# Optimization experiments

Hardware: AMD Instinct MI355X
Metric: run time of the kernel (lower is better)

Reference implementation:

```python
import jax, jax.numpy as jnp
import numpy as np

EPS = 1e-6

def feature_map(x):
    # 'elu' feature map: elu(x) + 1 (positive feature map from Katharopoulos et al.)
    return jax.nn.elu(x) + 1.0

def setup_inputs() -> dict:
    key = jax.random.key(0)
    kq, kk, kv = jax.random.split(key, 3)
    B, L, H, D = 4, 2048, 16, 64
    q = jax.random.normal(kq, (B, L, H, D), dtype=jnp.float32)
    k = jax.random.normal(kk, (B, L, H, D), dtype=jnp.float32)
    v = jax.random.normal(kv, (B, L, H, D), dtype=jnp.float32)
    return {"q": q, "k": k, "v": v}

def reference(q, k, v):
    # q, k, v: [N, L, H, D]  (attention_mask=None -> causal linear attention)
    qf = feature_map(q)
    kf = feature_map(k)
    # normalizer: z[n,l,h] = sum_d qf[n,l,h,d] * cumsum_s<=l kf[n,s,h,d]
    z = jnp.einsum('nlhd,nlhd->nlh', qf, jnp.cumsum(kf, axis=1)) + EPS
    # causal_dot_product via scan over sequence with carry S[n,h,d,m]
    B, L, H, D = q.shape
    M = v.shape[-1]
    qs = jnp.moveaxis(qf, 1, 0)  # [L, N, H, D]
    ks = jnp.moveaxis(kf, 1, 0)
    vs = jnp.moveaxis(v, 1, 0)

    def step(S, qkv):
        ql, kl, vl = qkv                              # [N,H,D], [N,H,D], [N,H,M]
        S = S + jnp.einsum('nhd,nhm->nhdm', kl, vl)   # running sum of k v^T
        out = jnp.einsum('nhd,nhdm->nhm', ql, S)
        return S, out

    S0 = jnp.zeros((B, H, D, M), dtype=q.dtype)
    _, outs = jax.lax.scan(step, S0, (qs, ks, vs))    # outs: [L, N, H, M]
    v_ = jnp.moveaxis(outs, 0, 1)                     # [N, L, H, M]
    return v_ / z[..., None]
```

## Files before the change

kernel.cpp:

```cpp
#include <hip/hip_runtime.h>
#include <cstdint>

#define LL 2048
#define HH 16
#define DD 64
#define LSTR 1024
#define EPSF 1e-6f
#define PAD 72

typedef __bf16 bf16x8 __attribute__((ext_vector_type(8)));
typedef float floatx4 __attribute__((ext_vector_type(4)));
typedef unsigned short ushortx8 __attribute__((ext_vector_type(8)));
typedef unsigned short ushortx4 __attribute__((ext_vector_type(4)));
typedef unsigned short ushortx2 __attribute__((ext_vector_type(2)));

static __device__ __forceinline__ float fmap(float x){ return x > 0.f ? x + 1.f : __expf(x); }
static __device__ __forceinline__ unsigned short f2bf(float f){
    unsigned u = __builtin_bit_cast(unsigned, f);
    u += 0x7fffu + ((u >> 16) & 1u);
    return (unsigned short)(u >> 16);
}
static __device__ __forceinline__ float bf2f(unsigned short s){
    unsigned u = ((unsigned)s) << 16;
    return __builtin_bit_cast(float, u);
}
static __device__ __forceinline__ bf16x8 ldf(const unsigned short* p){
    return __builtin_bit_cast(bf16x8, *(const ushortx8*)p);
}
static __device__ __forceinline__ float4 fmap4(float4 a){
    return float4{fmap(a.x), fmap(a.y), fmap(a.z), fmap(a.w)};
}

template<bool MAP>
static __device__ __forceinline__ void st_sd(unsigned short* base, int r, int c, float4 a, float4 b){
    if (MAP) {
        *(ushortx4*)(base + r*PAD + c)     = ushortx4{ f2bf(fmap(a.x)), f2bf(fmap(a.y)), f2bf(fmap(a.z)), f2bf(fmap(a.w)) };
        *(ushortx4*)(base + (r+1)*PAD + c) = ushortx4{ f2bf(fmap(b.x)), f2bf(fmap(b.y)), f2bf(fmap(b.z)), f2bf(fmap(b.w)) };
    } else {
        *(ushortx4*)(base + r*PAD + c)     = ushortx4{ f2bf(a.x), f2bf(a.y), f2bf(a.z), f2bf(a.w) };
        *(ushortx4*)(base + (r+1)*PAD + c) = ushortx4{ f2bf(b.x), f2bf(b.y), f2bf(b.z), f2bf(b.w) };
    }
}
template<bool MAP>
static __device__ __forceinline__ void st_tr(unsigned short* base, int r, int c, float4 a, float4 b){
    float aa[4] = {a.x, a.y, a.z, a.w}, bb[4] = {b.x, b.y, b.z, b.w};
#pragma unroll
    for (int e = 0; e < 4; ++e) {
        float x0 = MAP ? fmap(aa[e]) : aa[e];
        float x1 = MAP ? fmap(bb[e]) : bb[e];
        *(ushortx2*)(base + (c+e)*PAD + r) = ushortx2{ f2bf(x0), f2bf(x1) };
    }
}

__global__ __launch_bounds__(256) void kA(const float* __restrict__ kp, const float* __restrict__ vp,
                                          float* __restrict__ qkv, float* __restrict__ ksq)
{
    __shared__ __align__(16) unsigned short kft[2][DD*PAD];
    __shared__ __align__(16) unsigned short vtt[2][DD*PAD];
    const int blk = blockIdx.x;
    const int bh = blk >> 3, oct = blk & 7, b = bh >> 4, h = bh & 15;
    const int t = threadIdx.x;
    const int w = t >> 6, lane = t & 63, quad = lane >> 4, lr = lane & 15;
    const int m0 = 16*w;

    floatx4 acc[4];
#pragma unroll
    for (int dt = 0; dt < 4; ++dt) acc[dt] = floatx4{0.f,0.f,0.f,0.f};
    float ksa = 0.f;

    const int64_t gb0 = ((int64_t)(b*LL + oct*256)*HH + h)*DD;
#pragma unroll
    for (int ii = 0; ii < 2; ++ii) {
        int flat = t + 256*ii;
        int l0s = (flat >> 4) * 2, col4 = (flat & 15) << 2;
        const float* gk = kp + gb0 + (int64_t)l0s*LSTR + col4;
        const float* gv = vp + gb0 + (int64_t)l0s*LSTR + col4;
        float4 ka = *(const float4*)gk, kb = *(const float4*)(gk + LSTR);
        float4 va = *(const float4*)gv, vb = *(const float4*)(gv + LSTR);
        st_tr<true >(kft[0], l0s, col4, ka, kb);
        st_tr<false>(vtt[0], l0s, col4, va, vb);
    }
    __syncthreads();

#pragma unroll
    for (int sc = 0; sc < 4; ++sc) {
        const int p = sc & 1;
        float4 ka[2], kb[2], va[2], vb[2];
        if (sc < 3) {
            const int64_t gb = gb0 + (int64_t)(sc+1)*DD*LSTR;
#pragma unroll
            for (int ii = 0; ii < 2; ++ii) {
                int flat = t + 256*ii;
                int l0s = (flat >> 4) * 2, col4 = (flat & 15) << 2;
                const float* gk = kp + gb + (int64_t)l0s*LSTR + col4;
                const float* gv = vp + gb + (int64_t)l0s*LSTR + col4;
                ka[ii] = *(const float4*)gk; kb[ii] = *(const float4*)(gk + LSTR);
                va[ii] = *(const float4*)gv; vb[ii] = *(const float4*)(gv + LSTR);
            }
        }
#pragma unroll
        for (int kk = 0; kk < 2; ++kk) {
            bf16x8 a = ldf(vtt[p] + (m0+lr)*PAD + kk*32 + quad*8);
#pragma unroll
            for (int dt = 0; dt < 4; ++dt) {
                bf16x8 bbf = ldf(kft[p] + (dt*16+lr)*PAD + kk*32 + quad*8);
                acc[dt] = __builtin_amdgcn_mfma_f32_16x16x32_bf16(a, bbf, acc[dt], 0, 0, 0);
            }
        }
        if (t < DD) {
#pragma unroll
            for (int jj = 0; jj < 8; ++jj) {
                ushortx8 u = *(const ushortx8*)(kft[p] + t*PAD + jj*8);
#pragma unroll
                for (int e = 0; e < 8; ++e) ksa += bf2f(u[e]);
            }
        }
        if (sc < 3) {
#pragma unroll
            for (int ii = 0; ii < 2; ++ii) {
                int flat = t + 256*ii;
                int l0s = (flat >> 4) * 2, col4 = (flat & 15) << 2;
                st_tr<true >(kft[p^1], l0s, col4, ka[ii], kb[ii]);
                st_tr<false>(vtt[p^1], l0s, col4, va[ii], vb[ii]);
            }
        }
        __syncthreads();
    }

    float* qo = qkv + (int64_t)blk*4096;
#pragma unroll
    for (int dt = 0; dt < 4; ++dt)
#pragma unroll
        for (int r = 0; r < 4; ++r)
            qo[(m0 + quad*4 + r)*DD + dt*16 + lr] = acc[dt][r];
    if (t < DD) ksq[(int64_t)blk*DD + t] = ksa;
}

__global__ __launch_bounds__(512, 4) void kM(const float* __restrict__ qp, const float* __restrict__ kp,
                                             const float* __restrict__ vp,
                                             const float* __restrict__ qkv, const float* __restrict__ ksq,
                                             float* __restrict__ outp)
{
    __shared__ __align__(16) unsigned short qf [DD*PAD];
    __shared__ __align__(16) unsigned short kfx[DD*PAD];
    __shared__ __align__(16) unsigned short kft[DD*PAD];
    __shared__ __align__(16) unsigned short vtt[DD*PAD];
    __shared__ __align__(16) unsigned short sld[DD*PAD];
    __shared__ __align__(16) unsigned short sct[DD*PAD];
    __shared__ __align__(16) unsigned short kpx[16*PAD];
    __shared__ float ksum[DD];
    __shared__ float zp2[2][DD];

    const int bid = blockIdx.x;
    const int bh = bid >> 3, oct = bid & 7, b = bh >> 4, h = bh & 15;
    const int t = threadIdx.x;
    const int w = t >> 6, lane = t & 63, quad = lane >> 4, lr = lane & 15;
    const int wi = w >> 1, wj = w & 1;
    const int l0 = 16*wi;
    const int l0s = (t >> 4) * 2, col4 = (t & 15) << 2;

    const int64_t bhb = ((int64_t)b*LL*HH + h)*DD;
    const int cg0 = oct*4;

    if (t < 135) *(ushortx8*)(kpx + PAD + t*8) = ushortx8{0,0,0,0,0,0,0,0};
    const int no = oct;
    if (t < DD) {
        float s = 0.f;
        for (int o = 0; o < no; ++o) s += ksq[((int64_t)bh*8 + o)*DD + t];
        ksum[t] = s;
        kpx[t] = f2bf(s);
    }
    floatx4 S_acc[2];
    S_acc[0] = floatx4{0.f,0.f,0.f,0.f};
    S_acc[1] = floatx4{0.f,0.f,0.f,0.f};
    for (int o = 0; o < no; ++o) {
        const float* qo = qkv + ((int64_t)bh*8 + o)*4096;
#pragma unroll
        for (int dtl = 0; dtl < 2; ++dtl)
#pragma unroll
            for (int r = 0; r < 4; ++r)
                S_acc[dtl][r] += qo[(l0 + quad*4 + r)*DD + 32*wj + dtl*16 + lr];
    }
#pragma unroll
    for (int dtl = 0; dtl < 2; ++dtl)
#pragma unroll
        for (int r = 0; r < 4; ++r)
            sld[(l0 + quad*4 + r)*PAD + 32*wj + dtl*16 + lr] = f2bf(S_acc[dtl][r]);

    {
        const int64_t gb = bhb + (int64_t)cg0*DD*LSTR;
        const float* gq = qp + gb + (int64_t)l0s*LSTR + col4;
        const float* gk = kp + gb + (int64_t)l0s*LSTR + col4;
        const float* gv = vp + gb + (int64_t)l0s*LSTR + col4;
        float4 q0 = *(const float4*)gq, q1 = *(const float4*)(gq + LSTR);
        float4 k0 = *(const float4*)gk, k1 = *(const float4*)(gk + LSTR);
        float4 v0 = *(const float4*)gv, v1 = *(const float4*)(gv + LSTR);
        st_sd<true >(qf , l0s, col4, q0, q1);
        st_sd<true >(kfx, l0s, col4, k0, k1);
        st_tr<true >(kft, l0s, col4, k0, k1);
        st_tr<false>(vtt, l0s, col4, v0, v1);
    }
    __syncthreads();

    float4 lk0 = float4{0,0,0,0}, lk1 = float4{0,0,0,0};
    float4 lv0 = float4{0,0,0,0}, lv1 = float4{0,0,0,0};

#pragma unroll 2
    for (int c = 0; c < 4; ++c) {
        const int cg = cg0 + c;
        float4 nq0, nq1, nk0, nk1, nv0, nv1;
        if (c < 3) {
            const int64_t gb = bhb + (int64_t)(cg+1)*DD*LSTR;
            const float* gq = qp + gb + (int64_t)l0s*LSTR + col4;
            const float* gk = kp + gb + (int64_t)l0s*LSTR + col4;
            const float* gv = vp + gb + (int64_t)l0s*LSTR + col4;
            nq0 = *(const float4*)gq; nq1 = *(const float4*)(gq + LSTR);
            nk0 = *(const float4*)gk; nk1 = *(const float4*)(gk + LSTR);
            nv0 = *(const float4*)gv; nv1 = *(const float4*)(gv + LSTR);
        }
        if (c > 0) {
            st_tr<false>(kft, l0s, col4, lk0, lk1);
            st_tr<false>(vtt, l0s, col4, lv0, lv1);
        }
        bf16x8 aq0 = ldf(qf + (l0+lr)*PAD + quad*8);
        bf16x8 aq1 = ldf(qf + (l0+lr)*PAD + 32 + quad*8);
        bf16x8 bsf[2][2];
#pragma unroll
        for (int kk = 0; kk < 2; ++kk)
#pragma unroll
            for (int mt = 0; mt < 2; ++mt)
                bsf[kk][mt] = ldf(sld + ((2*wj+mt)*16+lr)*PAD + kk*32 + quad*8);
        floatx4 s0 = floatx4{0.f,0.f,0.f,0.f}, s1 = floatx4{0.f,0.f,0.f,0.f}, sp = floatx4{0.f,0.f,0.f,0.f};
#pragma unroll
        for (int kk = 0; kk < 2; ++kk) {
            bf16x8 aqk = kk ? aq1 : aq0;
            bf16x8 b0 = ldf(kfx + ((2*wj+0)*16+lr)*PAD + kk*32 + quad*8);
            bf16x8 b1 = ldf(kfx + ((2*wj+1)*16+lr)*PAD + kk*32 + quad*8);
            s0 = __builtin_amdgcn_mfma_f32_16x16x32_bf16(aqk, b0, s0, 0, 0, 0);
            s1 = __builtin_amdgcn_mfma_f32_16x16x32_bf16(aqk, b1, s1, 0, 0, 0);
            if (wj == 0) {
                bf16x8 bp = ldf(kpx + lr*PAD + kk*32 + quad*8);
                sp = __builtin_amdgcn_mfma_f32_16x16x32_bf16(aqk, bp, sp, 0, 0, 0);
            }
        }
        float zpv[4];
#pragma unroll
        for (int r = 0; r < 4; ++r) zpv[r] = (wj == 0 && lr == 0) ? sp[r] : 0.f;
#pragma unroll
        for (int tt = 0; tt < 2; ++tt) {
            int colb = (2*wj+tt)*16 + lr;
            floatx4 sv = tt ? s1 : s0;
#pragma unroll
            for (int r = 0; r < 4; ++r) {
                int row = l0 + quad*4 + r;
                float val = (colb <= row) ? sv[r] : 0.f;
                zpv[r] += val;
                sct[row*PAD + colb] = f2bf(val);
            }
        }
#pragma unroll
        for (int m = 1; m < 16; m <<= 1)
#pragma unroll
            for (int r = 0; r < 4; ++r) zpv[r] += __shfl_xor(zpv[r], m, 64);
        if (lr == 0) {
#pragma unroll
            for (int r = 0; r < 4; ++r) zp2[wj][l0 + quad*4 + r] = zpv[r];
        }
        __syncthreads();
        if (t < DD) {
            float s = ksum[t];
#pragma unroll
            for (int jj = 0; jj < 8; ++jj) {
                ushortx8 u = *(const ushortx8*)(kft + t*PAD + jj*8);
#pragma unroll
                for (int e = 0; e < 8; ++e) s += bf2f(u[e]);
            }
            ksum[t] = s;
            kpx[t] = f2bf(s);
        }
        floatx4 oa0 = floatx4{0.f,0.f,0.f,0.f}, oa1 = floatx4{0.f,0.f,0.f,0.f};
#pragma unroll
        for (int kk = 0; kk < 2; ++kk) {
            bf16x8 a2  = ldf(sct + (l0+lr)*PAD + kk*32 + quad*8);
            bf16x8 bv0 = ldf(vtt + ((2*wj+0)*16+lr)*PAD + kk*32 + quad*8);
            bf16x8 bv1 = ldf(vtt + ((2*wj+1)*16+lr)*PAD + kk*32 + quad*8);
            oa0 = __builtin_amdgcn_mfma_f32_16x16x32_bf16(a2, bv0, oa0, 0, 0, 0);
            oa1 = __builtin_amdgcn_mfma_f32_16x16x32_bf16(a2, bv1, oa1, 0, 0, 0);
        }
        oa0 = __builtin_amdgcn_mfma_f32_16x16x32_bf16(aq0, bsf[0][0], oa0, 0, 0, 0);
        oa0 = __builtin_amdgcn_mfma_f32_16x16x32_bf16(aq1, bsf[1][0], oa0, 0, 0, 0);
        oa1 = __builtin_amdgcn_mfma_f32_16x16x32_bf16(aq0, bsf[0][1], oa1, 0, 0, 0);
        oa1 = __builtin_amdgcn_mfma_f32_16x16x32_bf16(aq1, bsf[1][1], oa1, 0, 0, 0);
        {
            const int64_t ob = bhb + (int64_t)cg*DD*LSTR;
#pragma unroll
            for (int r = 0; r < 4; ++r) {
                int row = l0 + quad*4 + r;
                float rz = 1.f / (zp2[0][row] + zp2[1][row] + EPSF);
                outp[ob + (int64_t)row*LSTR + (2*wj+0)*16 + lr] = oa0[r] * rz;
                outp[ob + (int64_t)row*LSTR + (2*wj+1)*16 + lr] = oa1[r] * rz;
            }
        }
#pragma unroll
        for (int kk = 0; kk < 2; ++kk) {
            bf16x8 av = ldf(vtt + (l0+lr)*PAD + kk*32 + quad*8);
#pragma unroll
            for (int dtl = 0; dtl < 2; ++dtl) {
                bf16x8 bk = ldf(kft + ((2*wj+dtl)*16+lr)*PAD + kk*32 + quad*8);
                S_acc[dtl] = __builtin_amdgcn_mfma_f32_16x16x32_bf16(av, bk, S_acc[dtl], 0, 0, 0);
            }
        }
#pragma unroll
        for (int dtl = 0; dtl < 2; ++dtl)
#pragma unroll
            for (int r = 0; r < 4; ++r)
                sld[(l0 + quad*4 + r)*PAD + 32*wj + dtl*16 + lr] = f2bf(S_acc[dtl][r]);
        if (c < 3) {
            float4 fk0 = fmap4(nk0), fk1 = fmap4(nk1);
            st_sd<true >(qf , l0s, col4, nq0, nq1);
            st_sd<false>(kfx, l0s, col4, fk0, fk1);
            lk0 = fk0; lk1 = fk1; lv0 = nv0; lv1 = nv1;
        }
        __syncthreads();
    }
}

extern "C" void kernel_launch(void* const* d_in, const int* in_sizes, int n_in,
                              void* d_out, int out_size, void* d_ws, size_t ws_size,
                              hipStream_t stream) {
    const float* q = (const float*)d_in[0];
    const float* k = (const float*)d_in[1];
    const float* v = (const float*)d_in[2];
    float* out = (float*)d_out;
    float* qkv = (float*)d_ws;
    float* ksq = (float*)((char*)d_ws + (size_t)512*4096*4);
    kA<<<512, 256, 0, stream>>>(k, v, qkv, ksq);
    kM<<<512, 512, 0, stream>>>(q, k, v, qkv, ksq, out);
}
```

Before: 172.5 us.

## Swizzle transposed LDS tiles and double-buffer k/v transposes in main kernel

Applies an XOR swizzle to the transposed k and v shared-memory tiles, aiming to reduce bank conflicts on the strided transposed stores and MFMA operand loads. In the main kernel, the transposed k/v tiles become double-buffered, so the next chunk's transposed stores are issued at the end of the current iteration instead of at the start of the next. This removes the register carry of the previous chunk's k/v. It also lowers the launch-bounds occupancy hint from 4 to 2 and disables unrolling. The extra LDS for the double buffer may reduce occupancy.

```diff
diff --git a/kernel.cpp b/kernel.cpp
--- a/kernel.cpp
+++ b/kernel.cpp
@@ -7,6 +7,7 @@
 #define LSTR 1024
 #define EPSF 1e-6f
 #define PAD 72
+#define SWZ(row, off) ((row)*PAD + ((off) ^ ((((row)>>3)&7)<<3)))
 
 typedef __bf16 bf16x8 __attribute__((ext_vector_type(8)));
 typedef float floatx4 __attribute__((ext_vector_type(4)));
@@ -48,7 +49,7 @@
     for (int e = 0; e < 4; ++e) {
         float x0 = MAP ? fmap(aa[e]) : aa[e];
         float x1 = MAP ? fmap(bb[e]) : bb[e];
-        *(ushortx2*)(base + (c+e)*PAD + r) = ushortx2{ f2bf(x0), f2bf(x1) };
+        *(ushortx2*)(base + SWZ(c+e, r)) = ushortx2{ f2bf(x0), f2bf(x1) };
     }
 }
 
@@ -100,17 +101,17 @@
         }
 #pragma unroll
         for (int kk = 0; kk < 2; ++kk) {
-            bf16x8 a = ldf(vtt[p] + (m0+lr)*PAD + kk*32 + quad*8);
+            bf16x8 a = ldf(vtt[p] + SWZ(m0+lr, kk*32 + quad*8));
 #pragma unroll
             for (int dt = 0; dt < 4; ++dt) {
-                bf16x8 bbf = ldf(kft[p] + (dt*16+lr)*PAD + kk*32 + quad*8);
+                bf16x8 bbf = ldf(kft[p] + SWZ(dt*16+lr, kk*32 + quad*8));
                 acc[dt] = __builtin_amdgcn_mfma_f32_16x16x32_bf16(a, bbf, acc[dt], 0, 0, 0);
             }
         }
         if (t < DD) {
 #pragma unroll
             for (int jj = 0; jj < 8; ++jj) {
-                ushortx8 u = *(const ushortx8*)(kft[p] + t*PAD + jj*8);
+                ushortx8 u = *(const ushortx8*)(kft[p] + SWZ(t, jj*8));
 #pragma unroll
                 for (int e = 0; e < 8; ++e) ksa += bf2f(u[e]);
             }
@@ -136,15 +137,15 @@
     if (t < DD) ksq[(int64_t)blk*DD + t] = ksa;
 }
 
-__global__ __launch_bounds__(512, 4) void kM(const float* __restrict__ qp, const float* __restrict__ kp,
+__global__ __launch_bounds__(512, 2) void kM(const float* __restrict__ qp, const float* __restrict__ kp,
                                              const float* __restrict__ vp,
                                              const float* __restrict__ qkv, const float* __restrict__ ksq,
                                              float* __restrict__ outp)
 {
     __shared__ __align__(16) unsigned short qf [DD*PAD];
     __shared__ __align__(16) unsigned short kfx[DD*PAD];
-    __shared__ __align__(16) unsigned short kft[DD*PAD];
-    __shared__ __align__(16) unsigned short vtt[DD*PAD];
+    __shared__ __align__(16) unsigned short kftb[2][DD*PAD];
+    __shared__ __align__(16) unsigned short vttb[2][DD*PAD];
     __shared__ __align__(16) unsigned short sld[DD*PAD];
     __shared__ __align__(16) unsigned short sct[DD*PAD];
     __shared__ __align__(16) unsigned short kpx[16*PAD];
@@ -197,17 +198,16 @@
         float4 v0 = *(const float4*)gv, v1 = *(const float4*)(gv + LSTR);
         st_sd<true >(qf , l0s, col4, q0, q1);
         st_sd<true >(kfx, l0s, col4, k0, k1);
-        st_tr<true >(kft, l0s, col4, k0, k1);
-        st_tr<false>(vtt, l0s, col4, v0, v1);
+        st_tr<true >(kftb[0], l0s, col4, k0, k1);
+        st_tr<false>(vttb[0], l0s, col4, v0, v1);
     }
     __syncthreads();
 
-    float4 lk0 = float4{0,0,0,0}, lk1 = float4{0,0,0,0};
-    float4 lv0 = float4{0,0,0,0}, lv1 = float4{0,0,0,0};
-
-#pragma unroll 2
+#pragma unroll 1
     for (int c = 0; c < 4; ++c) {
         const int cg = cg0 + c;
+        const unsigned short* kftc = kftb[c & 1];
+        const unsigned short* vttc = vttb[c & 1];
         float4 nq0, nq1, nk0, nk1, nv0, nv1;
         if (c < 3) {
             const int64_t gb = bhb + (int64_t)(cg+1)*DD*LSTR;
@@ -218,10 +218,6 @@
             nk0 = *(const float4*)gk; nk1 = *(const float4*)(gk + LSTR);
             nv0 = *(const float4*)gv; nv1 = *(const float4*)(gv + LSTR);
         }
-        if (c > 0) {
-            st_tr<false>(kft, l0s, col4, lk0, lk1);
-            st_tr<false>(vtt, l0s, col4, lv0, lv1);
-        }
         bf16x8 aq0 = ldf(qf + (l0+lr)*PAD + quad*8);
         bf16x8 aq1 = ldf(qf + (l0+lr)*PAD + 32 + quad*8);
         bf16x8 bsf[2][2];
@@ -271,7 +267,7 @@
             float s = ksum[t];
 #pragma unroll
             for (int jj = 0; jj < 8; ++jj) {
-                ushortx8 u = *(const ushortx8*)(kft + t*PAD + jj*8);
+                ushortx8 u = *(const ushortx8*)(kftc + SWZ(t, jj*8));
 #pragma unroll
                 for (int e = 0; e < 8; ++e) s += bf2f(u[e]);
             }
@@ -282,8 +278,8 @@
 #pragma unroll
         for (int kk = 0; kk < 2; ++kk) {
             bf16x8 a2  = ldf(sct + (l0+lr)*PAD + kk*32 + quad*8);
-            bf16x8 bv0 = ldf(vtt + ((2*wj+0)*16+lr)*PAD + kk*32 + quad*8);
-            bf16x8 bv1 = ldf(vtt + ((2*wj+1)*16+lr)*PAD + kk*32 + quad*8);
+            bf16x8 bv0 = ldf(vttc + SWZ((2*wj+0)*16+lr, kk*32 + quad*8));
+            bf16x8 bv1 = ldf(vttc + SWZ((2*wj+1)*16+lr, kk*32 + quad*8));
             oa0 = __builtin_amdgcn_mfma_f32_16x16x32_bf16(a2, bv0, oa0, 0, 0, 0);
             oa1 = __builtin_amdgcn_mfma_f32_16x16x32_bf16(a2, bv1, oa1, 0, 0, 0);
         }
@@ -303,10 +299,10 @@
         }
 #pragma unroll
         for (int kk = 0; kk < 2; ++kk) {
-            bf16x8 av = ldf(vtt + (l0+lr)*PAD + kk*32 + quad*8);
+            bf16x8 av = ldf(vttc + SWZ(l0+lr, kk*32 + quad*8));
 #pragma unroll
             for (int dtl = 0; dtl < 2; ++dtl) {
-                bf16x8 bk = ldf(kft + ((2*wj+dtl)*16+lr)*PAD + kk*32 + quad*8);
+                bf16x8 bk = ldf(kftc + SWZ((2*wj+dtl)*16+lr, kk*32 + quad*8));
                 S_acc[dtl] = __builtin_amdgcn_mfma_f32_16x16x32_bf16(av, bk, S_acc[dtl], 0, 0, 0);
             }
         }
@@ -319,7 +315,8 @@
             float4 fk0 = fmap4(nk0), fk1 = fmap4(nk1);
             st_sd<true >(qf , l0s, col4, nq0, nq1);
             st_sd<false>(kfx, l0s, col4, fk0, fk1);
-            lk0 = fk0; lk1 = fk1; lv0 = nv0; lv1 = nv1;
+            st_tr<false>(kftb[(c+1)&1], l0s, col4, fk0, fk1);
+            st_tr<false>(vttb[(c+1)&1], l0s, col4, nv0, nv1);
         }
         __syncthreads();
     }
```

Result: faster. 155.8 us (-9.7%).
